# Performance work log

Hardware: AMD Instinct MI355X
Metric: run time of the kernel (lower is better)

Reference implementation:

```python
import jax, jax.numpy as jnp
import numpy as np


def _squash(t):
    # squash along axis=2 (the atoms axis of [B, D, A, 1, 1])
    norm = jnp.linalg.norm(t, axis=2, keepdims=True)
    n2 = norm * norm
    return t / norm * (n2 / (1.0 + n2))


def setup_inputs() -> dict:
    key = jax.random.key(0)
    k1, k2 = jax.random.split(key)
    B, I, Ain, D, A = 32, 2048, 16, 32, 16
    x = jax.random.normal(k1, (B, I, Ain, 1, 1), jnp.float32)
    weights = 0.1 * jax.random.normal(k2, (I, Ain, D * A, 1, 1), jnp.float32)
    bias = jnp.full((D, A, 1, 1), 0.1, jnp.float32)  # nn.init.constant_(0.1)
    return {"x": x, "weights": weights, "bias": bias, "num_routing": 3}


def reference(x, weights, bias, num_routing):
    B, I, Ain = x.shape[:3]
    D, A = bias.shape[:2]
    # Vote computation (standard voting): sum over input_atoms.
    # Torch does expand+mul+sum; einsum is the same math without the 4.8GB intermediate.
    votes = jnp.einsum('bia,iao->bio', x[:, :, :, 0, 0],
                       weights[:, :, :, 0, 0]).reshape(B, I, D, A, 1, 1)
    votes_sg = jax.lax.stop_gradient(votes)  # votes_trans_stopped in torch
    logits = jnp.zeros((B, I, D, 1, 1), x.dtype)
    activation = None
    for i in range(num_routing):
        route = jax.nn.softmax(logits, axis=2)  # [B, I, D, 1, 1], softmax over D
        v = votes if i == num_routing - 1 else votes_sg
        # route broadcast over atoms axis; sum over input capsules I
        preact = jnp.sum(route[:, :, :, None] * v, axis=1) + bias  # [B, D, A, 1, 1]
        activation = _squash(preact)
        if i < num_routing - 1:
            # agreement update uses non-stopped votes (as in torch)
            logits = logits + jnp.sum(votes * activation[:, None], axis=3)  # [B, I, D, 1, 1]
    return activation
```

## Files before the change

### kernel.cpp

```cpp
#include <hip/hip_runtime.h>


#define B_  32
#define I_  2048
#define K_  16
#define O_  512
#define NG_ 256
#define IC_ 8

#define GLB(p)  ((const __attribute__((address_space(1))) void*)(p))
#define LDSP(p) ((__attribute__((address_space(3))) void*)(p))

template<int PASS>
__global__ __launch_bounds__(256, 2)
void sweep_kernel(const float* __restrict__ x, const float* __restrict__ W,
                  const float* __restrict__ act0_g, const float* __restrict__ act1_g,
                  float* __restrict__ partial)
{
    const int tid  = threadIdx.x;
    const int lane = tid & 63;
    const int wave = tid >> 6;
    const int bid  = blockIdx.x;
    const int ig   = (bid & 7) * 32 + (bid >> 4);
    const int bh   = (bid >> 3) & 1;
    const int d    = lane >> 1;
    const int h    = lane & 1;
    const int obase = d * 16 + h * 8;

    const int wv    = __builtin_amdgcn_readfirstlane(wave);
    const int bbase = bh * 16 + wv * 4;

    __shared__ float sW[2][K_ * O_];

    int voff[8];
    #pragma unroll
    for (int c = 0; c < 8; ++c) {
        const int s = c * 256 + wave * 64 + lane;
        const int f = ((s >> 10) & 1) | ((s & 1) << 1)
                    | (((s >> 1) & 31) << 2) | (((s >> 6) & 15) << 7);
        voff[c] = f << 4;
    }

    float facc[4][8];
    #pragma unroll
    for (int bb = 0; bb < 4; ++bb)
        #pragma unroll
        for (int j = 0; j < 8; ++j) facc[bb][j] = 0.f;

    float as_[4][8];
    if (PASS >= 1) {
        #pragma unroll
        for (int bb = 0; bb < 4; ++bb) {
            const float4* p = (const float4*)(act0_g + (bbase + bb) * O_ + obase);
            float4 f0 = p[0], f1 = p[1];
            as_[bb][0]=f0.x; as_[bb][1]=f0.y; as_[bb][2]=f0.z; as_[bb][3]=f0.w;
            as_[bb][4]=f1.x; as_[bb][5]=f1.y; as_[bb][6]=f1.z; as_[bb][7]=f1.w;
            if (PASS == 2) {
                const float4* q = (const float4*)(act1_g + (bbase + bb) * O_ + obase);
                float4 g0 = q[0], g1 = q[1];
                as_[bb][0]+=g0.x; as_[bb][1]+=g0.y; as_[bb][2]+=g0.z; as_[bb][3]+=g0.w;
                as_[bb][4]+=g1.x; as_[bb][5]+=g1.y; as_[bb][6]+=g1.z; as_[bb][7]+=g1.w;
            }
        }
    }

    {
        const char* gb = (const char*)(W + (size_t)(ig * IC_) * (K_ * O_));
        #pragma unroll
        for (int c = 0; c < 8; ++c)
            __builtin_amdgcn_global_load_lds(GLB(gb + voff[c]),
                LDSP(&sW[0][(c * 256 + wave * 64) * 4]), 16, 0, 0);
    }

    #pragma unroll 1
    for (int ii = 0; ii < IC_; ++ii) {
        const int i = ig * IC_ + ii;
        __syncthreads();
        if (ii + 1 < IC_) {
            const char* gb = (const char*)(W + (size_t)(i + 1) * (K_ * O_));
            float* nbuf = sW[(ii + 1) & 1];
            #pragma unroll
            for (int c = 0; c < 8; ++c)
                __builtin_amdgcn_global_load_lds(GLB(gb + voff[c]),
                    LDSP(&nbuf[(c * 256 + wave * 64) * 4]), 16, 0, 0);
        }
        const float* cbuf = sW[ii & 1];

        float xs[4][16];
        #pragma unroll
        for (int bb = 0; bb < 4; ++bb) {
            const float4* xp = (const float4*)(x + ((size_t)(bbase + bb) * I_ + i) * K_);
            #pragma unroll
            for (int q = 0; q < 4; ++q) {
                float4 v = xp[q];
                xs[bb][4*q+0]=v.x; xs[bb][4*q+1]=v.y; xs[bb][4*q+2]=v.z; xs[bb][4*q+3]=v.w;
            }
        }

        float V[4][8];
        #pragma unroll
        for (int bb = 0; bb < 4; ++bb)
            #pragma unroll
            for (int j = 0; j < 8; ++j) V[bb][j] = 0.f;

        #pragma unroll
        for (int kh = 0; kh < 2; ++kh) {
            float4 wr0[8], wr1[8];
            #pragma unroll
            for (int kq = 0; kq < 8; ++kq) {
                const int k = kh * 8 + kq;
                wr0[kq] = *(const float4*)&cbuf[k * 256 + lane * 4];
                wr1[kq] = *(const float4*)&cbuf[4096 + k * 256 + lane * 4];
            }
            #pragma unroll
            for (int kq = 0; kq < 8; ++kq) {
                const int k = kh * 8 + kq;
                const float w[8] = {wr0[kq].x, wr0[kq].y, wr0[kq].z, wr0[kq].w,
                                    wr1[kq].x, wr1[kq].y, wr1[kq].z, wr1[kq].w};
                #pragma unroll
                for (int bb = 0; bb < 4; ++bb) {
                    const float xb = xs[bb][k];
                    #pragma unroll
                    for (int j = 0; j < 8; ++j) V[bb][j] = fmaf(xb, w[j], V[bb][j]);
                }
            }
        }

        #pragma unroll
        for (int bb = 0; bb < 4; ++bb) {
            if (PASS == 0) {
                #pragma unroll
                for (int j = 0; j < 8; ++j) facc[bb][j] += V[bb][j];
            } else {
                float p0 = 0.f;
                #pragma unroll
                for (int j = 0; j < 8; ++j) p0 = fmaf(V[bb][j], as_[bb][j], p0);
                p0 += __shfl_xor(p0, 1);
                const float e = __expf(p0);
                float s = e;
                s += __shfl_xor(s, 2);
                s += __shfl_xor(s, 4);
                s += __shfl_xor(s, 8);
                s += __shfl_xor(s, 16);
                s += __shfl_xor(s, 32);
                const float r = e * __builtin_amdgcn_rcpf(s);
                #pragma unroll
                for (int j = 0; j < 8; ++j)
                    facc[bb][j] = fmaf(r, V[bb][j], facc[bb][j]);
            }
        }
    }

    #pragma unroll
    for (int bb = 0; bb < 4; ++bb) {
        const int b = bbase + bb;
        float4* dst = (float4*)(partial + ((size_t)ig * B_ + b) * O_ + obase);
        dst[0] = make_float4(facc[bb][0], facc[bb][1], facc[bb][2], facc[bb][3]);
        dst[1] = make_float4(facc[bb][4], facc[bb][5], facc[bb][6], facc[bb][7]);
    }
}

__global__ __launch_bounds__(256)
void reduce_squash(const float* __restrict__ partial, const float* __restrict__ bias,
                   float scale, float* __restrict__ out)
{
    const int t  = threadIdx.x;
    const int g  = blockIdx.x * 32 + (t & 31);
    const int sl = t >> 5;
    float s = 0.f;
    #pragma unroll
    for (int w = sl * 32; w < sl * 32 + 32; ++w)
        s += partial[(size_t)w * (B_ * O_) + g];
    __shared__ float red[256];
    red[t] = s;
    __syncthreads();
    if (t < 32) {
        float v = red[t];
        #pragma unroll
        for (int r = 1; r < 8; ++r) v += red[t + 32 * r];
        const float p = fmaf(v, scale, bias[g & (O_ - 1)]);
        float nn = p * p;
        nn += __shfl_xor(nn, 1);
        nn += __shfl_xor(nn, 2);
        nn += __shfl_xor(nn, 4);
        nn += __shfl_xor(nn, 8);
        out[g] = p * sqrtf(nn) / (1.f + nn);
    }
}

extern "C" void kernel_launch(void* const* d_in, const int* in_sizes, int n_in,
                              void* d_out, int out_size, void* d_ws, size_t ws_size,
                              hipStream_t stream) {
    const float* x    = (const float*)d_in[0];
    const float* W    = (const float*)d_in[1];
    const float* bias = (const float*)d_in[2];
    float* out = (float*)d_out;

    float* partial = (float*)d_ws;
    float* act0    = partial + (size_t)NG_ * B_ * O_;
    float* act1    = act0 + B_ * O_;

    sweep_kernel<0><<<NG_ * 2, 256, 0, stream>>>(x, W, nullptr, nullptr, partial);
    reduce_squash<<<512, 256, 0, stream>>>(partial, bias, 1.f / 32.f, act0);
    sweep_kernel<1><<<NG_ * 2, 256, 0, stream>>>(x, W, act0, nullptr, partial);
    reduce_squash<<<512, 256, 0, stream>>>(partial, bias, 1.f, act1);
    sweep_kernel<2><<<NG_ * 2, 256, 0, stream>>>(x, W, act0, act1, partial);
    reduce_squash<<<512, 256, 0, stream>>>(partial, bias, 1.f, out);
}
```

Baseline: 186.5 us.

## Deepen weight-tile prefetch to two stages and prefetch next x into registers

```diff
diff --git a/kernel.cpp b/kernel.cpp
--- a/kernel.cpp
+++ b/kernel.cpp
@@ -64,38 +64,39 @@
         }
     }
 
+    const size_t igbase = (size_t)(ig * IC_) * (K_ * O_);
+
+    float xs[4][16];
     {
-        const char* gb = (const char*)(W + (size_t)(ig * IC_) * (K_ * O_));
-        #pragma unroll
-        for (int c = 0; c < 8; ++c)
-            __builtin_amdgcn_global_load_lds(GLB(gb + voff[c]),
-                LDSP(&sW[0][(c * 256 + wave * 64) * 4]), 16, 0, 0);
-    }
+        const int i = ig * IC_;
+        #pragma unroll
+        for (int bb = 0; bb < 4; ++bb) {
+            const float4* xp = (const float4*)(x + ((size_t)(bbase + bb) * I_ + i) * K_);
+            #pragma unroll
+            for (int q = 0; q < 4; ++q) {
+                float4 v = xp[q];
+                xs[bb][4*q+0]=v.x; xs[bb][4*q+1]=v.y; xs[bb][4*q+2]=v.z; xs[bb][4*q+3]=v.w;
+            }
+        }
+    }
+
+    #pragma unroll
+    for (int c = 0; c < 8; ++c)
+        __builtin_amdgcn_global_load_lds(GLB((const char*)(W) + igbase * 4 + voff[c]),
+            LDSP(&sW[0][(c * 256 + wave * 64) * 4]), 16, 0, 0);
+    #pragma unroll
+    for (int c = 0; c < 8; ++c)
+        __builtin_amdgcn_global_load_lds(GLB((const char*)(W) + (igbase + K_ * O_) * 4 + voff[c]),
+            LDSP(&sW[1][(c * 256 + wave * 64) * 4]), 16, 0, 0);
+    asm volatile("s_waitcnt vmcnt(8)" ::: "memory");
+    __builtin_amdgcn_sched_barrier(0);
+    __builtin_amdgcn_s_barrier();
+    __builtin_amdgcn_sched_barrier(0);
 
     #pragma unroll 1
     for (int ii = 0; ii < IC_; ++ii) {
         const int i = ig * IC_ + ii;
-        __syncthreads();
-        if (ii + 1 < IC_) {
-            const char* gb = (const char*)(W + (size_t)(i + 1) * (K_ * O_));
-            float* nbuf = sW[(ii + 1) & 1];
-            #pragma unroll
-            for (int c = 0; c < 8; ++c)
-                __builtin_amdgcn_global_load_lds(GLB(gb + voff[c]),
-                    LDSP(&nbuf[(c * 256 + wave * 64) * 4]), 16, 0, 0);
-        }
         const float* cbuf = sW[ii & 1];
-
-        float xs[4][16];
-        #pragma unroll
-        for (int bb = 0; bb < 4; ++bb) {
-            const float4* xp = (const float4*)(x + ((size_t)(bbase + bb) * I_ + i) * K_);
-            #pragma unroll
-            for (int q = 0; q < 4; ++q) {
-                float4 v = xp[q];
-                xs[bb][4*q+0]=v.x; xs[bb][4*q+1]=v.y; xs[bb][4*q+2]=v.z; xs[bb][4*q+3]=v.w;
-            }
-        }
 
         float V[4][8];
         #pragma unroll
@@ -125,6 +126,35 @@
                 }
             }
         }
+
+        if (ii + 1 < IC_) {
+            #pragma unroll
+            for (int bb = 0; bb < 4; ++bb) {
+                const float4* xp = (const float4*)(x + ((size_t)(bbase + bb) * I_ + (i + 1)) * K_);
+                #pragma unroll
+                for (int q = 0; q < 4; ++q) {
+                    float4 v = xp[q];
+                    xs[bb][4*q+0]=v.x; xs[bb][4*q+1]=v.y; xs[bb][4*q+2]=v.z; xs[bb][4*q+3]=v.w;
+                }
+            }
+        }
+
+        __builtin_amdgcn_s_barrier();
+        __builtin_amdgcn_sched_barrier(0);
+        if (ii + 2 < IC_) {
+            const char* gb = (const char*)(W + igbase + (size_t)(ii + 2) * (K_ * O_));
+            float* nbuf = sW[ii & 1];
+            #pragma unroll
+            for (int c = 0; c < 8; ++c)
+                __builtin_amdgcn_global_load_lds(GLB(gb + voff[c]),
+                    LDSP(&nbuf[(c * 256 + wave * 64) * 4]), 16, 0, 0);
+            asm volatile("s_waitcnt vmcnt(8)" ::: "memory");
+        } else {
+            asm volatile("s_waitcnt vmcnt(0)" ::: "memory");
+        }
+        __builtin_amdgcn_sched_barrier(0);
+        __builtin_amdgcn_s_barrier();
+        __builtin_amdgcn_sched_barrier(0);
 
         #pragma unroll
         for (int bb = 0; bb < 4; ++bb) {
```

After: 200.2 us. 7.4% more time.
